# Optimization experiments

Hardware: AMD Instinct MI355X
Metric: run time of the kernel (lower is better)

Reference implementation:

```python
import jax, jax.numpy as jnp
import numpy as np

ADIM = 128
VDIM = 64

def setup_inputs() -> dict:
    key = jax.random.key(0)
    ks = jax.random.split(key, 12)
    B, N, E = 4, 10000, 320000
    pos_0 = jax.random.normal(ks[0], (B, N, 3), dtype=jnp.float32)
    pos_1 = jax.random.normal(ks[1], (B, N, 3), dtype=jnp.float32)
    src = jax.random.randint(ks[2], (E,), 0, N, dtype=jnp.int64)
    dst = jax.random.randint(ks[3], (E,), 0, N, dtype=jnp.int64)
    # parameters (torch default inits approximated; randn for VecLinear as in source)
    Wv = jax.random.normal(ks[4], (VDIM, 6), dtype=jnp.float32)
    def lin(k, fan_in, fan_out):
        kw, kb = jax.random.split(k)
        bound = 1.0 / np.sqrt(fan_in)
        W = jax.random.uniform(kw, (fan_out, fan_in), minval=-bound, maxval=bound, dtype=jnp.float32)
        b = jax.random.uniform(kb, (fan_out,), minval=-bound, maxval=bound, dtype=jnp.float32)
        return W, b
    W1, b1 = lin(ks[5], 6, ADIM)
    W2, b2 = lin(ks[6], ADIM, ADIM)
    W3, b3 = lin(ks[7], ADIM, ADIM)
    return {"pos_0": pos_0, "pos_1": pos_1, "src": src, "dst": dst,
            "Wv": Wv, "W1": W1, "b1": b1, "W2": W2, "b2": b2, "W3": W3, "b3": b3}

def _leaky(x):
    return jnp.where(x >= 0, x, 0.2 * x)

def reference(pos_0, pos_1, src, dst, Wv, W1, b1, W2, b2, W3, b3):
    # gather endpoint positions: (B, E, 3)
    p0s = jnp.take(pos_0, src, axis=1)
    p0d = jnp.take(pos_0, dst, axis=1)
    p1s = jnp.take(pos_1, src, axis=1)
    p1d = jnp.take(pos_1, dst, axis=1)
    # 6 relative vectors: (B, E, 6, 3)
    vecs = jnp.stack([p0d - p0s, p1d - p1s, p1s - p0s, p1d - p0d, p1s - p0d, p1d - p0s], axis=2)
    norms = jnp.sqrt(jnp.sum(vecs * vecs, axis=-1))  # (B, E, 6)
    h = _leaky(jnp.einsum('bei,oi->beo', norms, W1) + b1)
    h = _leaky(jnp.einsum('bei,oi->beo', h, W2) + b2)
    a_out = jnp.einsum('bei,oi->beo', h, W3) + b3  # (B, E, ADIM)
    v_out = jnp.einsum('oi,beik->beok', Wv, vecs) / 3  # (B, E, VDIM, 3)
    return (a_out, v_out)
```

## Files before the change

kernel.cpp:

```cpp
#include <hip/hip_runtime.h>

#define NB 4
#define NN 10000
#define NE 320000
#define EPB 64
#define NBLK ((NB * NE) / EPB)

typedef unsigned int uint;
typedef unsigned short ushort;
typedef __attribute__((ext_vector_type(8))) short short8;
typedef __attribute__((ext_vector_type(4))) float f32x4;

#define WS_W1T 0
#define WS_W2T 8192
#define WS_W3T 40960
#define WS_WVT 73728

static __device__ __forceinline__ ushort f2bf(float f) {
    uint u = __float_as_uint(f);
    u += 0x7fffu + ((u >> 16) & 1u);
    return (ushort)(u >> 16);
}
static __device__ __forceinline__ uint pack2(float a, float b) {
    return (uint)f2bf(a) | ((uint)f2bf(b) << 16);
}
static __device__ __forceinline__ short8 u4s8(uint4 v) {
    union { uint4 u; short8 s; } x; x.u = v; return x.s;
}
static __device__ __forceinline__ float lk(float x) { return x >= 0.f ? x : 0.2f * x; }

__global__ void prep_kernel(const float* __restrict__ W1, const float* __restrict__ W2,
                            const float* __restrict__ W3, const float* __restrict__ Wv,
                            unsigned char* __restrict__ ws) {
    int tid = blockIdx.x * blockDim.x + threadIdx.x;
    if (tid < 4096) {
        const float* W = (tid < 2048) ? W2 : W3;
        uint4* dst = (uint4*)(ws + ((tid < 2048) ? WS_W2T : WS_W3T));
        int f = tid & 2047;
        int lane = f & 63, kt = (f >> 6) & 3, mt = (f >> 8) & 7;
        int la = lane >> 4, lm = lane & 15;
        int n = mt * 16 + lm;
        uint w[4];
        #pragma unroll
        for (int jw = 0; jw < 4; ++jw) {
            int j0 = jw * 2, j1 = j0 + 1;
            int k0 = kt * 32 + (j0 >> 2) * 16 + la * 4 + (j0 & 3);
            int k1 = kt * 32 + (j1 >> 2) * 16 + la * 4 + (j1 & 3);
            w[jw] = pack2(W[n * 128 + k0], W[n * 128 + k1]);
        }
        dst[f] = make_uint4(w[0], w[1], w[2], w[3]);
    } else if (tid < 4608) {
        int f = tid - 4096;
        int lane = f & 63, mt = f >> 6;
        int la = lane >> 4, lm = lane & 15;
        int n = mt * 16 + lm;
        uint w[4];
        #pragma unroll
        for (int jw = 0; jw < 4; ++jw) {
            int j0 = jw * 2, j1 = j0 + 1;
            int k0 = (j0 >> 2) * 16 + la * 4 + (j0 & 3);
            int k1 = (j1 >> 2) * 16 + la * 4 + (j1 & 3);
            float f0 = (k0 < 6) ? W1[n * 6 + k0] : 0.f;
            float f1 = (k1 < 6) ? W1[n * 6 + k1] : 0.f;
            w[jw] = pack2(f0, f1);
        }
        ((uint4*)(ws + WS_W1T))[f] = make_uint4(w[0], w[1], w[2], w[3]);
    } else if (tid < 5376) {
        int f = tid - 4608;
        int lane = f & 63, mt = f >> 6;
        int la = lane >> 4, lm = lane & 15;
        int row = mt * 16 + lm;
        int o = row / 3, c = row - o * 3;
        uint w[4];
        #pragma unroll
        for (int jw = 0; jw < 4; ++jw) {
            float vv[2];
            #pragma unroll
            for (int dc = 0; dc < 2; ++dc) {
                int j = jw * 2 + dc;
                int k = (j >> 2) * 16 + la * 4 + (j & 3);
                int i = k / 3, cc = k - i * 3;
                vv[dc] = (k < 18 && cc == c) ? Wv[o * 6 + i] * (1.f / 3.f) : 0.f;
            }
            w[jw] = pack2(vv[0], vv[1]);
        }
        ((uint4*)(ws + WS_WVT))[f] = make_uint4(w[0], w[1], w[2], w[3]);
    }
}

__global__ __launch_bounds__(256, 3)
void edge_kernel(const float* __restrict__ pos0, const float* __restrict__ pos1,
                 const int* __restrict__ src, const int* __restrict__ dstI,
                 const float* __restrict__ b1, const float* __restrict__ b2,
                 const float* __restrict__ b3,
                 const unsigned char* __restrict__ ws, float* __restrict__ out) {
    __shared__ float s_pts[64][13];
    __shared__ float s_vecs[64][20];
    __shared__ float s_norms[8][64];
    __shared__ uint4 s_B[16 * 64];

    const int tid = threadIdx.x;
    const int lane = tid & 63;
    const int wid = tid >> 6;
    const int wm = wid & 1;
    const int wn = wid >> 1;
    const int lm = lane & 15;
    const int la = lane >> 4;

    const int bid = blockIdx.x;
    const int b = bid / (NE / EPB);
    const int e0 = (bid % (NE / EPB)) * EPB;
    const size_t eg0 = (size_t)b * NE + e0;

    const uint4* W1T = (const uint4*)(ws + WS_W1T);
    const uint4* W2T = (const uint4*)(ws + WS_W2T);
    const uint4* W3T = (const uint4*)(ws + WS_W3T);
    const uint4* WVT = (const uint4*)(ws + WS_WVT);

    {
        int le = tid & 63;
        int pt = tid >> 6;
        int e = e0 + le;
        int node = (pt & 1) ? dstI[e] : src[e];
        const float* P = (pt < 2) ? pos0 : pos1;
        const float* p = P + ((size_t)b * NN + node) * 3;
        s_pts[le][pt * 3 + 0] = p[0];
        s_pts[le][pt * 3 + 1] = p[1];
        s_pts[le][pt * 3 + 2] = p[2];
    }
    __syncthreads();

    {
        const int row = tid & 63;
        const int w = tid >> 6;
        if (w == 0) {
            float P[12];
            #pragma unroll
            for (int i = 0; i < 12; ++i) P[i] = s_pts[row][i];
            const int va[4] = {1, 3, 2, 3}, vb_[4] = {0, 2, 0, 1};
            float v[4][3];
            #pragma unroll
            for (int i = 0; i < 4; ++i) {
                #pragma unroll
                for (int c = 0; c < 3; ++c) v[i][c] = P[va[i] * 3 + c] - P[vb_[i] * 3 + c];
                s_norms[i][row] = sqrtf(v[i][0]*v[i][0] + v[i][1]*v[i][1] + v[i][2]*v[i][2]);
            }
            float4 t0 = {v[0][0], v[0][1], v[0][2], v[1][0]};
            float4 t1 = {v[1][1], v[1][2], v[2][0], v[2][1]};
            float4 t2 = {v[2][2], v[3][0], v[3][1], v[3][2]};
            *(float4*)&s_vecs[row][0] = t0;
            *(float4*)&s_vecs[row][4] = t1;
            *(float4*)&s_vecs[row][8] = t2;
        } else if (w == 1) {
            float P[12];
            #pragma unroll
            for (int i = 0; i < 12; ++i) P[i] = s_pts[row][i];
            float v4[3], v5[3];
            #pragma unroll
            for (int c = 0; c < 3; ++c) {
                v4[c] = P[6 + c] - P[3 + c];
                v5[c] = P[9 + c] - P[0 + c];
            }
            s_norms[4][row] = sqrtf(v4[0]*v4[0] + v4[1]*v4[1] + v4[2]*v4[2]);
            s_norms[5][row] = sqrtf(v5[0]*v5[0] + v5[1]*v5[1] + v5[2]*v5[2]);
            float4 t = {v4[0], v4[1], v4[2], v5[0]};
            *(float4*)&s_vecs[row][12] = t;
            float2 t2 = {v5[1], v5[2]};
            *(float2*)&s_vecs[row][16] = t2;
        }
    }
    __syncthreads();

    const f32x4 zero4 = {0.f, 0.f, 0.f, 0.f};
    f32x4 acc[4][2];

    {
        uint4 vb1[2];
        #pragma unroll
        for (int nt = 0; nt < 2; ++nt) {
            int e = (wn * 2 + nt) * 16 + lm;
            uint c0 = 0, c1 = 0;
            if (la == 0) {
                c0 = pack2(s_norms[0][e], s_norms[1][e]);
                c1 = pack2(s_norms[2][e], s_norms[3][e]);
            } else if (la == 1) {
                c0 = pack2(s_norms[4][e], s_norms[5][e]);
            }
            vb1[nt] = make_uint4(c0, c1, 0u, 0u);
        }
        uint4 w1f[4];
        #pragma unroll
        for (int mtl = 0; mtl < 4; ++mtl) w1f[mtl] = W1T[(wm * 4 + mtl) * 64 + lane];
        #pragma unroll
        for (int mtl = 0; mtl < 4; ++mtl)
            #pragma unroll
            for (int nt = 0; nt < 2; ++nt)
                acc[mtl][nt] = __builtin_amdgcn_mfma_f32_16x16x32_bf16(
                    u4s8(w1f[mtl]), u4s8(vb1[nt]), zero4, 0, 0, 0);
    }
    #pragma unroll
    for (int mtl = 0; mtl < 4; ++mtl) {
        float4 bc = *(const float4*)&b1[(wm * 4 + mtl) * 16 + la * 4];
        #pragma unroll
        for (int nt = 0; nt < 2; ++nt) {
            acc[mtl][nt][0] = lk(acc[mtl][nt][0] + bc.x);
            acc[mtl][nt][1] = lk(acc[mtl][nt][1] + bc.y);
            acc[mtl][nt][2] = lk(acc[mtl][nt][2] + bc.z);
            acc[mtl][nt][3] = lk(acc[mtl][nt][3] + bc.w);
        }
    }
    #pragma unroll
    for (int nt = 0; nt < 2; ++nt)
        #pragma unroll
        for (int t = 0; t < 2; ++t) {
            f32x4 ha = acc[2 * t][nt], hb = acc[2 * t + 1][nt];
            s_B[((wn * 2 + nt) * 4 + wm * 2 + t) * 64 + lane] =
                make_uint4(pack2(ha[0], ha[1]), pack2(ha[2], ha[3]),
                           pack2(hb[0], hb[1]), pack2(hb[2], hb[3]));
        }
    __syncthreads();

    uint4 vb[2][4];
    #pragma unroll
    for (int nt = 0; nt < 2; ++nt)
        #pragma unroll
        for (int kt = 0; kt < 4; ++kt)
            vb[nt][kt] = s_B[((wn * 2 + nt) * 4 + kt) * 64 + lane];
    __syncthreads();

    {
        uint4 wf[4][4];
        #pragma unroll
        for (int mtl = 0; mtl < 4; ++mtl)
            #pragma unroll
            for (int kt = 0; kt < 4; ++kt)
                wf[mtl][kt] = W2T[((wm * 4 + mtl) * 4 + kt) * 64 + lane];
        #pragma unroll
        for (int mtl = 0; mtl < 4; ++mtl)
            #pragma unroll
            for (int nt = 0; nt < 2; ++nt) acc[mtl][nt] = zero4;
        #pragma unroll
        for (int kt = 0; kt < 4; ++kt)
            #pragma unroll
            for (int mtl = 0; mtl < 4; ++mtl)
                #pragma unroll
                for (int nt = 0; nt < 2; ++nt)
                    acc[mtl][nt] = __builtin_amdgcn_mfma_f32_16x16x32_bf16(
                        u4s8(wf[mtl][kt]), u4s8(vb[nt][kt]), acc[mtl][nt], 0, 0, 0);
    }
    #pragma unroll
    for (int mtl = 0; mtl < 4; ++mtl) {
        float4 bc = *(const float4*)&b2[(wm * 4 + mtl) * 16 + la * 4];
        #pragma unroll
        for (int nt = 0; nt < 2; ++nt) {
            acc[mtl][nt][0] = lk(acc[mtl][nt][0] + bc.x);
            acc[mtl][nt][1] = lk(acc[mtl][nt][1] + bc.y);
            acc[mtl][nt][2] = lk(acc[mtl][nt][2] + bc.z);
            acc[mtl][nt][3] = lk(acc[mtl][nt][3] + bc.w);
        }
    }
    #pragma unroll
    for (int nt = 0; nt < 2; ++nt)
        #pragma unroll
        for (int t = 0; t < 2; ++t) {
            f32x4 ha = acc[2 * t][nt], hb = acc[2 * t + 1][nt];
            s_B[((wn * 2 + nt) * 4 + wm * 2 + t) * 64 + lane] =
                make_uint4(pack2(ha[0], ha[1]), pack2(ha[2], ha[3]),
                           pack2(hb[0], hb[1]), pack2(hb[2], hb[3]));
        }
    __syncthreads();

    #pragma unroll
    for (int nt = 0; nt < 2; ++nt)
        #pragma unroll
        for (int kt = 0; kt < 4; ++kt)
            vb[nt][kt] = s_B[((wn * 2 + nt) * 4 + kt) * 64 + lane];

    {
        uint4 wf[4][4];
        #pragma unroll
        for (int mtl = 0; mtl < 4; ++mtl)
            #pragma unroll
            for (int kt = 0; kt < 4; ++kt)
                wf[mtl][kt] = W3T[((wm * 4 + mtl) * 4 + kt) * 64 + lane];
        #pragma unroll
        for (int mtl = 0; mtl < 4; ++mtl)
            #pragma unroll
            for (int nt = 0; nt < 2; ++nt) acc[mtl][nt] = zero4;
        #pragma unroll
        for (int kt = 0; kt < 4; ++kt)
            #pragma unroll
            for (int mtl = 0; mtl < 4; ++mtl)
                #pragma unroll
                for (int nt = 0; nt < 2; ++nt)
                    acc[mtl][nt] = __builtin_amdgcn_mfma_f32_16x16x32_bf16(
                        u4s8(wf[mtl][kt]), u4s8(vb[nt][kt]), acc[mtl][nt], 0, 0, 0);
    }
    #pragma unroll
    for (int mtl = 0; mtl < 4; ++mtl) {
        float4 bc = *(const float4*)&b3[(wm * 4 + mtl) * 16 + la * 4];
        #pragma unroll
        for (int nt = 0; nt < 2; ++nt) {
            float4 v = {acc[mtl][nt][0] + bc.x, acc[mtl][nt][1] + bc.y,
                        acc[mtl][nt][2] + bc.z, acc[mtl][nt][3] + bc.w};
            size_t e = eg0 + (wn * 2 + nt) * 16 + lm;
            *(float4*)&out[e * 128 + (wm * 4 + mtl) * 16 + la * 4] = v;
        }
    }

    {
        uint4 vbv[2];
        #pragma unroll
        for (int nt = 0; nt < 2; ++nt) {
            int e = (wn * 2 + nt) * 16 + lm;
            int base = la * 4;
            uint c0 = pack2(s_vecs[e][base], s_vecs[e][base + 1]);
            uint c1 = pack2(s_vecs[e][base + 2], s_vecs[e][base + 3]);
            uint c2 = (la == 0) ? pack2(s_vecs[e][16], s_vecs[e][17]) : 0u;
            vbv[nt] = make_uint4(c0, c1, c2, 0u);
        }
        float* vout = out + (size_t)NB * NE * 128;
        #pragma unroll
        for (int m6 = 0; m6 < 6; ++m6) {
            uint4 wv = WVT[(wm * 6 + m6) * 64 + lane];
            #pragma unroll
            for (int nt = 0; nt < 2; ++nt) {
                f32x4 av = __builtin_amdgcn_mfma_f32_16x16x32_bf16(
                    u4s8(wv), u4s8(vbv[nt]), zero4, 0, 0, 0);
                size_t e = eg0 + (wn * 2 + nt) * 16 + lm;
                float4 v = {av[0], av[1], av[2], av[3]};
                *(float4*)&vout[e * 192 + (wm * 6 + m6) * 16 + la * 4] = v;
            }
        }
    }
}

extern "C" void kernel_launch(void* const* d_in, const int* in_sizes, int n_in,
                              void* d_out, int out_size, void* d_ws, size_t ws_size,
                              hipStream_t stream) {
    const float* pos0 = (const float*)d_in[0];
    const float* pos1 = (const float*)d_in[1];
    const int* src = (const int*)d_in[2];
    const int* dstI = (const int*)d_in[3];
    const float* Wv = (const float*)d_in[4];
    const float* W1 = (const float*)d_in[5];
    const float* b1 = (const float*)d_in[6];
    const float* W2 = (const float*)d_in[7];
    const float* b2 = (const float*)d_in[8];
    const float* W3 = (const float*)d_in[9];
    const float* b3 = (const float*)d_in[10];
    unsigned char* ws = (unsigned char*)d_ws;
    float* out = (float*)d_out;

    prep_kernel<<<dim3(21), dim3(256), 0, stream>>>(W1, W2, W3, Wv, ws);
    edge_kernel<<<dim3(NBLK), dim3(256), 0, stream>>>(pos0, pos1, src, dstI, b1, b2, b3, ws, out);
}
```

Baseline: 442.1 us.

## Make each wave own 32 edges end-to-end, removing LDS exchanges and barriers

```diff
diff --git a/kernel.cpp b/kernel.cpp
--- a/kernel.cpp
+++ b/kernel.cpp
@@ -3,7 +3,7 @@
 #define NB 4
 #define NN 10000
 #define NE 320000
-#define EPB 64
+#define EPB 128
 #define NBLK ((NB * NE) / EPB)
 
 typedef unsigned int uint;
@@ -24,10 +24,17 @@
 static __device__ __forceinline__ uint pack2(float a, float b) {
     return (uint)f2bf(a) | ((uint)f2bf(b) << 16);
 }
+static __device__ __forceinline__ uint cvtpk(float a, float b) {
+    uint r;
+    asm("v_cvt_pk_bf16_f32 %0, %1, %2" : "=v"(r) : "v"(a), "v"(b));
+    return r;
+}
 static __device__ __forceinline__ short8 u4s8(uint4 v) {
     union { uint4 u; short8 s; } x; x.u = v; return x.s;
 }
-static __device__ __forceinline__ float lk(float x) { return x >= 0.f ? x : 0.2f * x; }
+static __device__ __forceinline__ f32x4 MF(uint4 a, uint4 b, f32x4 c) {
+    return __builtin_amdgcn_mfma_f32_16x16x32_bf16(u4s8(a), u4s8(b), c, 0, 0, 0);
+}
 
 __global__ void prep_kernel(const float* __restrict__ W1, const float* __restrict__ W2,
                             const float* __restrict__ W3, const float* __restrict__ Wv,
@@ -94,18 +101,16 @@
                  const float* __restrict__ b1, const float* __restrict__ b2,
                  const float* __restrict__ b3,
                  const unsigned char* __restrict__ ws, float* __restrict__ out) {
-    __shared__ float s_pts[64][13];
-    __shared__ float s_vecs[64][20];
-    __shared__ float s_norms[8][64];
-    __shared__ uint4 s_B[16 * 64];
+    __shared__ float s_pts[128][13];
+    __shared__ float s_vecs[128][20];
+    __shared__ float s_norms[6][128];
 
     const int tid = threadIdx.x;
     const int lane = tid & 63;
-    const int wid = tid >> 6;
-    const int wm = wid & 1;
-    const int wn = wid >> 1;
+    const int w = tid >> 6;
     const int lm = lane & 15;
     const int la = lane >> 4;
+    const int ew0 = w * 32;
 
     const int bid = blockIdx.x;
     const int b = bid / (NE / EPB);
@@ -118,219 +123,189 @@
     const uint4* WVT = (const uint4*)(ws + WS_WVT);
 
     {
-        int le = tid & 63;
-        int pt = tid >> 6;
-        int e = e0 + le;
-        int node = (pt & 1) ? dstI[e] : src[e];
-        const float* P = (pt < 2) ? pos0 : pos1;
-        const float* p = P + ((size_t)b * NN + node) * 3;
-        s_pts[le][pt * 3 + 0] = p[0];
-        s_pts[le][pt * 3 + 1] = p[1];
-        s_pts[le][pt * 3 + 2] = p[2];
-    }
-    __syncthreads();
+        const int el = ew0 + (lane & 31);
+        const int side = lane >> 5;
+        const int e = e0 + el;
+        const int node = side ? dstI[e] : src[e];
+        const size_t pb = ((size_t)b * NN + node) * 3;
+        float a0 = pos0[pb], a1 = pos0[pb + 1], a2 = pos0[pb + 2];
+        float c0 = pos1[pb], c1 = pos1[pb + 1], c2 = pos1[pb + 2];
+        s_pts[el][side * 3 + 0] = a0;
+        s_pts[el][side * 3 + 1] = a1;
+        s_pts[el][side * 3 + 2] = a2;
+        s_pts[el][6 + side * 3 + 0] = c0;
+        s_pts[el][6 + side * 3 + 1] = c1;
+        s_pts[el][6 + side * 3 + 2] = c2;
+    }
 
     {
-        const int row = tid & 63;
-        const int w = tid >> 6;
-        if (w == 0) {
-            float P[12];
-            #pragma unroll
-            for (int i = 0; i < 12; ++i) P[i] = s_pts[row][i];
-            const int va[4] = {1, 3, 2, 3}, vb_[4] = {0, 2, 0, 1};
+        const int el = ew0 + (lane & 31);
+        const int grp = lane >> 5;
+        float P[12];
+        #pragma unroll
+        for (int i = 0; i < 12; ++i) P[i] = s_pts[el][i];
+        if (grp == 0) {
+            const int va[4] = {1, 3, 2, 3}, vbx[4] = {0, 2, 0, 1};
             float v[4][3];
             #pragma unroll
             for (int i = 0; i < 4; ++i) {
                 #pragma unroll
-                for (int c = 0; c < 3; ++c) v[i][c] = P[va[i] * 3 + c] - P[vb_[i] * 3 + c];
-                s_norms[i][row] = sqrtf(v[i][0]*v[i][0] + v[i][1]*v[i][1] + v[i][2]*v[i][2]);
+                for (int c = 0; c < 3; ++c) v[i][c] = P[va[i] * 3 + c] - P[vbx[i] * 3 + c];
+                s_norms[i][el] = sqrtf(v[i][0]*v[i][0] + v[i][1]*v[i][1] + v[i][2]*v[i][2]);
             }
             float4 t0 = {v[0][0], v[0][1], v[0][2], v[1][0]};
             float4 t1 = {v[1][1], v[1][2], v[2][0], v[2][1]};
             float4 t2 = {v[2][2], v[3][0], v[3][1], v[3][2]};
-            *(float4*)&s_vecs[row][0] = t0;
-            *(float4*)&s_vecs[row][4] = t1;
-            *(float4*)&s_vecs[row][8] = t2;
-        } else if (w == 1) {
-            float P[12];
-            #pragma unroll
-            for (int i = 0; i < 12; ++i) P[i] = s_pts[row][i];
+            *(float4*)&s_vecs[el][0] = t0;
+            *(float4*)&s_vecs[el][4] = t1;
+            *(float4*)&s_vecs[el][8] = t2;
+        } else {
             float v4[3], v5[3];
             #pragma unroll
             for (int c = 0; c < 3; ++c) {
                 v4[c] = P[6 + c] - P[3 + c];
                 v5[c] = P[9 + c] - P[0 + c];
             }
-            s_norms[4][row] = sqrtf(v4[0]*v4[0] + v4[1]*v4[1] + v4[2]*v4[2]);
-            s_norms[5][row] = sqrtf(v5[0]*v5[0] + v5[1]*v5[1] + v5[2]*v5[2]);
+            s_norms[4][el] = sqrtf(v4[0]*v4[0] + v4[1]*v4[1] + v4[2]*v4[2]);
+            s_norms[5][el] = sqrtf(v5[0]*v5[0] + v5[1]*v5[1] + v5[2]*v5[2]);
             float4 t = {v4[0], v4[1], v4[2], v5[0]};
-            *(float4*)&s_vecs[row][12] = t;
+            *(float4*)&s_vecs[el][12] = t;
             float2 t2 = {v5[1], v5[2]};
-            *(float2*)&s_vecs[row][16] = t2;
-        }
-    }
-    __syncthreads();
+            *(float2*)&s_vecs[el][16] = t2;
+        }
+    }
 
     const f32x4 zero4 = {0.f, 0.f, 0.f, 0.f};
-    f32x4 acc[4][2];
-
+
+    {
+        uint4 vbv[2];
+        #pragma unroll
+        for (int nt = 0; nt < 2; ++nt) {
+            const int e = ew0 + nt * 16 + lm;
+            float4 q = *(const float4*)&s_vecs[e][la * 4];
+            uint c2 = 0;
+            if (la == 0) c2 = cvtpk(s_vecs[e][16], s_vecs[e][17]);
+            vbv[nt] = make_uint4(cvtpk(q.x, q.y), cvtpk(q.z, q.w), c2, 0u);
+        }
+        uint4 wv[12];
+        #pragma unroll
+        for (int mt = 0; mt < 12; ++mt) wv[mt] = WVT[mt * 64 + lane];
+        float* vout = out + (size_t)NB * NE * 128;
+        #pragma unroll
+        for (int mt = 0; mt < 12; ++mt)
+            #pragma unroll
+            for (int nt = 0; nt < 2; ++nt) {
+                f32x4 av = MF(wv[mt], vbv[nt], zero4);
+                const size_t e = eg0 + ew0 + nt * 16 + lm;
+                *(f32x4*)&vout[e * 192 + mt * 16 + la * 4] = av;
+            }
+    }
+
+    f32x4 acc[8][2];
     {
         uint4 vb1[2];
         #pragma unroll
         for (int nt = 0; nt < 2; ++nt) {
-            int e = (wn * 2 + nt) * 16 + lm;
+            const int e = ew0 + nt * 16 + lm;
             uint c0 = 0, c1 = 0;
             if (la == 0) {
-                c0 = pack2(s_norms[0][e], s_norms[1][e]);
-                c1 = pack2(s_norms[2][e], s_norms[3][e]);
+                c0 = cvtpk(s_norms[0][e], s_norms[1][e]);
+                c1 = cvtpk(s_norms[2][e], s_norms[3][e]);
             } else if (la == 1) {
-                c0 = pack2(s_norms[4][e], s_norms[5][e]);
+                c0 = cvtpk(s_norms[4][e], s_norms[5][e]);
             }
             vb1[nt] = make_uint4(c0, c1, 0u, 0u);
         }
-        uint4 w1f[4];
-        #pragma unroll
-        for (int mtl = 0; mtl < 4; ++mtl) w1f[mtl] = W1T[(wm * 4 + mtl) * 64 + lane];
-        #pragma unroll
-        for (int mtl = 0; mtl < 4; ++mtl)
+        uint4 w1f[8];
+        #pragma unroll
+        for (int mt = 0; mt < 8; ++mt) w1f[mt] = W1T[mt * 64 + lane];
+        #pragma unroll
+        for (int mt = 0; mt < 8; ++mt)
             #pragma unroll
             for (int nt = 0; nt < 2; ++nt)
-                acc[mtl][nt] = __builtin_amdgcn_mfma_f32_16x16x32_bf16(
-                    u4s8(w1f[mtl]), u4s8(vb1[nt]), zero4, 0, 0, 0);
-    }
-    #pragma unroll
-    for (int mtl = 0; mtl < 4; ++mtl) {
-        float4 bc = *(const float4*)&b1[(wm * 4 + mtl) * 16 + la * 4];
+                acc[mt][nt] = MF(w1f[mt], vb1[nt], zero4);
+    }
+    uint4 vb[2][4];
+    #pragma unroll
+    for (int mt = 0; mt < 8; ++mt) {
+        f32x4 bc = *(const f32x4*)&b1[mt * 16 + la * 4];
+        #pragma unroll
+        for (int nt = 0; nt < 2; ++nt)
+            #pragma unroll
+            for (int r = 0; r < 4; ++r) {
+                float x = acc[mt][nt][r] + bc[r];
+                acc[mt][nt][r] = fmaxf(x, 0.2f * x);
+            }
+    }
+    #pragma unroll
+    for (int nt = 0; nt < 2; ++nt)
+        #pragma unroll
+        for (int kt = 0; kt < 4; ++kt)
+            vb[nt][kt] = make_uint4(
+                cvtpk(acc[2*kt][nt][0], acc[2*kt][nt][1]),
+                cvtpk(acc[2*kt][nt][2], acc[2*kt][nt][3]),
+                cvtpk(acc[2*kt+1][nt][0], acc[2*kt+1][nt][1]),
+                cvtpk(acc[2*kt+1][nt][2], acc[2*kt+1][nt][3]));
+
+    #pragma unroll
+    for (int mt = 0; mt < 8; ++mt)
+        #pragma unroll
+        for (int nt = 0; nt < 2; ++nt) acc[mt][nt] = zero4;
+    #pragma unroll
+    for (int kt = 0; kt < 4; ++kt) {
+        uint4 wf[8];
+        #pragma unroll
+        for (int mt = 0; mt < 8; ++mt) wf[mt] = W2T[(mt * 4 + kt) * 64 + lane];
+        #pragma unroll
+        for (int mt = 0; mt < 8; ++mt)
+            #pragma unroll
+            for (int nt = 0; nt < 2; ++nt)
+                acc[mt][nt] = MF(wf[mt], vb[nt][kt], acc[mt][nt]);
+    }
+    #pragma unroll
+    for (int mt = 0; mt < 8; ++mt) {
+        f32x4 bc = *(const f32x4*)&b2[mt * 16 + la * 4];
+        #pragma unroll
+        for (int nt = 0; nt < 2; ++nt)
+            #pragma unroll
+            for (int r = 0; r < 4; ++r) {
+                float x = acc[mt][nt][r] + bc[r];
+                acc[mt][nt][r] = fmaxf(x, 0.2f * x);
+            }
+    }
+    #pragma unroll
+    for (int nt = 0; nt < 2; ++nt)
+        #pragma unroll
+        for (int kt = 0; kt < 4; ++kt)
+            vb[nt][kt] = make_uint4(
+                cvtpk(acc[2*kt][nt][0], acc[2*kt][nt][1]),
+                cvtpk(acc[2*kt][nt][2], acc[2*kt][nt][3]),
+                cvtpk(acc[2*kt+1][nt][0], acc[2*kt+1][nt][1]),
+                cvtpk(acc[2*kt+1][nt][2], acc[2*kt+1][nt][3]));
+
+    #pragma unroll
+    for (int mt = 0; mt < 8; ++mt)
+        #pragma unroll
+        for (int nt = 0; nt < 2; ++nt) acc[mt][nt] = zero4;
+    #pragma unroll
+    for (int kt = 0; kt < 4; ++kt) {
+        uint4 wf[8];
+        #pragma unroll
+        for (int mt = 0; mt < 8; ++mt) wf[mt] = W3T[(mt * 4 + kt) * 64 + lane];
+        #pragma unroll
+        for (int mt = 0; mt < 8; ++mt)
+            #pragma unroll
+            for (int nt = 0; nt < 2; ++nt)
+                acc[mt][nt] = MF(wf[mt], vb[nt][kt], acc[mt][nt]);
+    }
+    #pragma unroll
+    for (int mt = 0; mt < 8; ++mt) {
+        f32x4 bc = *(const f32x4*)&b3[mt * 16 + la * 4];
         #pragma unroll
         for (int nt = 0; nt < 2; ++nt) {
-            acc[mtl][nt][0] = lk(acc[mtl][nt][0] + bc.x);
-            acc[mtl][nt][1] = lk(acc[mtl][nt][1] + bc.y);
-            acc[mtl][nt][2] = lk(acc[mtl][nt][2] + bc.z);
-            acc[mtl][nt][3] = lk(acc[mtl][nt][3] + bc.w);
-        }
-    }
-    #pragma unroll
-    for (int nt = 0; nt < 2; ++nt)
-        #pragma unroll
-        for (int t = 0; t < 2; ++t) {
-            f32x4 ha = acc[2 * t][nt], hb = acc[2 * t + 1][nt];
-            s_B[((wn * 2 + nt) * 4 + wm * 2 + t) * 64 + lane] =
-                make_uint4(pack2(ha[0], ha[1]), pack2(ha[2], ha[3]),
-                           pack2(hb[0], hb[1]), pack2(hb[2], hb[3]));
-        }
-    __syncthreads();
-
-    uint4 vb[2][4];
-    #pragma unroll
-    for (int nt = 0; nt < 2; ++nt)
-        #pragma unroll
-        for (int kt = 0; kt < 4; ++kt)
-            vb[nt][kt] = s_B[((wn * 2 + nt) * 4 + kt) * 64 + lane];
-    __syncthreads();
-
-    {
-        uint4 wf[4][4];
-        #pragma unroll
-        for (int mtl = 0; mtl < 4; ++mtl)
-            #pragma unroll
-            for (int kt = 0; kt < 4; ++kt)
-                wf[mtl][kt] = W2T[((wm * 4 + mtl) * 4 + kt) * 64 + lane];
-        #pragma unroll
-        for (int mtl = 0; mtl < 4; ++mtl)
-            #pragma unroll
-            for (int nt = 0; nt < 2; ++nt) acc[mtl][nt] = zero4;
-        #pragma unroll
-        for (int kt = 0; kt < 4; ++kt)
-            #pragma unroll
-            for (int mtl = 0; mtl < 4; ++mtl)
-                #pragma unroll
-                for (int nt = 0; nt < 2; ++nt)
-                    acc[mtl][nt] = __builtin_amdgcn_mfma_f32_16x16x32_bf16(
-                        u4s8(wf[mtl][kt]), u4s8(vb[nt][kt]), acc[mtl][nt], 0, 0, 0);
-    }
-    #pragma unroll
-    for (int mtl = 0; mtl < 4; ++mtl) {
-        float4 bc = *(const float4*)&b2[(wm * 4 + mtl) * 16 + la * 4];
-        #pragma unroll
-        for (int nt = 0; nt < 2; ++nt) {
-            acc[mtl][nt][0] = lk(acc[mtl][nt][0] + bc.x);
-            acc[mtl][nt][1] = lk(acc[mtl][nt][1] + bc.y);
-            acc[mtl][nt][2] = lk(acc[mtl][nt][2] + bc.z);
-            acc[mtl][nt][3] = lk(acc[mtl][nt][3] + bc.w);
-        }
-    }
-    #pragma unroll
-    for (int nt = 0; nt < 2; ++nt)
-        #pragma unroll
-        for (int t = 0; t < 2; ++t) {
-            f32x4 ha = acc[2 * t][nt], hb = acc[2 * t + 1][nt];
-            s_B[((wn * 2 + nt) * 4 + wm * 2 + t) * 64 + lane] =
-                make_uint4(pack2(ha[0], ha[1]), pack2(ha[2], ha[3]),
-                           pack2(hb[0], hb[1]), pack2(hb[2], hb[3]));
-        }
-    __syncthreads();
-
-    #pragma unroll
-    for (int nt = 0; nt < 2; ++nt)
-        #pragma unroll
-        for (int kt = 0; kt < 4; ++kt)
-            vb[nt][kt] = s_B[((wn * 2 + nt) * 4 + kt) * 64 + lane];
-
-    {
-        uint4 wf[4][4];
-        #pragma unroll
-        for (int mtl = 0; mtl < 4; ++mtl)
-            #pragma unroll
-            for (int kt = 0; kt < 4; ++kt)
-                wf[mtl][kt] = W3T[((wm * 4 + mtl) * 4 + kt) * 64 + lane];
-        #pragma unroll
-        for (int mtl = 0; mtl < 4; ++mtl)
-            #pragma unroll
-            for (int nt = 0; nt < 2; ++nt) acc[mtl][nt] = zero4;
-        #pragma unroll
-        for (int kt = 0; kt < 4; ++kt)
-            #pragma unroll
-            for (int mtl = 0; mtl < 4; ++mtl)
-                #pragma unroll
-                for (int nt = 0; nt < 2; ++nt)
-                    acc[mtl][nt] = __builtin_amdgcn_mfma_f32_16x16x32_bf16(
-                        u4s8(wf[mtl][kt]), u4s8(vb[nt][kt]), acc[mtl][nt], 0, 0, 0);
-    }
-    #pragma unroll
-    for (int mtl = 0; mtl < 4; ++mtl) {
-        float4 bc = *(const float4*)&b3[(wm * 4 + mtl) * 16 + la * 4];
-        #pragma unroll
-        for (int nt = 0; nt < 2; ++nt) {
-            float4 v = {acc[mtl][nt][0] + bc.x, acc[mtl][nt][1] + bc.y,
-                        acc[mtl][nt][2] + bc.z, acc[mtl][nt][3] + bc.w};
-            size_t e = eg0 + (wn * 2 + nt) * 16 + lm;
-            *(float4*)&out[e * 128 + (wm * 4 + mtl) * 16 + la * 4] = v;
-        }
-    }
-
-    {
-        uint4 vbv[2];
-        #pragma unroll
-        for (int nt = 0; nt < 2; ++nt) {
-            int e = (wn * 2 + nt) * 16 + lm;
-            int base = la * 4;
-            uint c0 = pack2(s_vecs[e][base], s_vecs[e][base + 1]);
-            uint c1 = pack2(s_vecs[e][base + 2], s_vecs[e][base + 3]);
-            uint c2 = (la == 0) ? pack2(s_vecs[e][16], s_vecs[e][17]) : 0u;
-            vbv[nt] = make_uint4(c0, c1, c2, 0u);
-        }
-        float* vout = out + (size_t)NB * NE * 128;
-        #pragma unroll
-        for (int m6 = 0; m6 < 6; ++m6) {
-            uint4 wv = WVT[(wm * 6 + m6) * 64 + lane];
-            #pragma unroll
-            for (int nt = 0; nt < 2; ++nt) {
-                f32x4 av = __builtin_amdgcn_mfma_f32_16x16x32_bf16(
-                    u4s8(wv), u4s8(vbv[nt]), zero4, 0, 0, 0);
-                size_t e = eg0 + (wn * 2 + nt) * 16 + lm;
-                float4 v = {av[0], av[1], av[2], av[3]};
-                *(float4*)&vout[e * 192 + (wm * 6 + m6) * 16 + la * 4] = v;
-            }
+            f32x4 v = acc[mt][nt] + bc;
+            const size_t e = eg0 + ew0 + nt * 16 + lm;
+            *(f32x4*)&out[e * 128 + mt * 16 + la * 4] = v;
         }
     }
 }
```

Result: no change. 435.8 us (-1.4%).
